# Kernel tuning notes

Hardware: AMD Instinct MI355X
Metric: run time of the kernel (lower is better)

The kernel has to match this reference:

```python
import jax, jax.numpy as jnp
import numpy as np

DOWN = 8
N_CLASSES = 80
IOU_THRESH = 0.7
ALL_ANCHORS = np.array([[10, 13], [16, 30], [33, 23], [30, 61], [62, 45],
                        [59, 119], [116, 90], [156, 198], [373, 326]],
                       np.float32) / DOWN              # anchors in grid units
ANCHOR_IDX = np.array([0, 1, 2])
ANCHORS = ALL_ANCHORS[ANCHOR_IDX]                       # [A,2]
A = 3
NC = N_CLASSES + 5


def _clog(z):
    # torch BCE clamps log at -100; double-where keeps grads finite at z==0
    safe = jnp.where(z > 0, z, 1.0)
    return jnp.where(z > 0, jnp.clip(jnp.log(safe), -100.0, None), -100.0)


def _bce_sum(p, t, w=None):
    term = t * _clog(p) + (1.0 - t) * _clog(1.0 - p)
    if w is not None:
        term = term * w
    return -jnp.sum(term)


def reference(x, targets, conv_w, conv_b):
    B, Cin, F, _ = x.shape
    T = targets.shape[1]
    anchors = jnp.asarray(ANCHORS)
    all_anchors = jnp.asarray(ALL_ANCHORS)

    # 1x1 conv + axis swap -> [B, A, Fy, Fx, NC]
    out = jnp.einsum('bchw,oc->bohw', x, conv_w) + conv_b[None, :, None, None]
    out = out.reshape(B, A, NC, F, F).transpose(0, 1, 3, 4, 2)
    sig = jax.nn.sigmoid(out)
    outputs = jnp.concatenate([sig[..., :2], out[..., 2:4], sig[..., 4:]], axis=-1)

    # decoded predicted boxes (detached), grid units
    gr = jnp.arange(F, dtype=outputs.dtype)
    grid = jnp.stack([jnp.broadcast_to(gr[None, :], (F, F)),
                      jnp.broadcast_to(gr[:, None], (F, F))], -1)   # (x,y)
    pred_xy = outputs[..., :2] + grid[None, None]
    pred_wh = jnp.exp(outputs[..., 2:4]) * anchors[None, :, None, None, :]
    pred_boxes = jax.lax.stop_gradient(jnp.concatenate([pred_xy, pred_wh], -1))

    # ground truth in grid units; valid targets are packed first (sum > 0)
    valid = jnp.sum(targets, axis=2) > 0                 # [B,T]
    n_t = jnp.sum(valid.astype(jnp.int32), axis=1)       # [B]
    gt_boxes = targets[..., :4] * F
    gt_cls = targets[..., 4].astype(jnp.int32)
    gxi = gt_boxes[..., 0].astype(jnp.int32)
    gyi = gt_boxes[..., 1].astype(jnp.int32)

    # best-matching anchor per gt (shape-only IoU vs all 9 anchors)
    wh = gt_boxes[..., 2:4]
    inter = jnp.prod(jnp.minimum(wh[:, :, None, :], all_anchors[None, None]), -1)
    union = (jnp.prod(wh, -1)[:, :, None]
             + jnp.prod(all_anchors, -1)[None, None] - inter)
    best = jnp.argmax(inter / (union + 1e-16), axis=2)   # [B,T]
    match = best[:, :, None] == jnp.asarray(ANCHOR_IDX)[None, None, :]
    keep = valid & jnp.any(match, -1)
    la = jnp.where(keep, jnp.argmax(match, -1), A)       # A == out-of-bounds -> drop

    # ignore predictions whose best IoU against any valid gt exceeds threshold
    p = pred_boxes.reshape(B, -1, 1, 4)                  # [B, A*F*F, 1, 4]
    g = gt_boxes[:, None, :, :]                          # [B, 1, T, 4]
    lo = jnp.maximum(p[..., :2] - p[..., 2:] * 0.5, g[..., :2] - g[..., 2:] * 0.5)
    hi = jnp.minimum(p[..., :2] + p[..., 2:] * 0.5, g[..., :2] + g[..., 2:] * 0.5)
    ia = jnp.prod(jnp.clip(hi - lo, 0.0, None), -1)
    iou = ia / (jnp.prod(p[..., 2:], -1) + jnp.prod(g[..., 2:], -1) - ia + 1e-16)
    iou = jnp.where(valid[:, None, :], iou, 0.0)
    high = (jnp.max(iou, -1) > IOU_THRESH).reshape(B, A, F, F).astype(outputs.dtype)
    a_rng = jnp.arange(A)
    object_mask = jnp.where(a_rng[None, :, None, None] < n_t[:, None, None, None],
                            1.0 - high, jnp.ones((), outputs.dtype))

    # scatter gt assignments (unique grid cells per image in setup -> no dup writes)
    bidx = jnp.broadcast_to(jnp.arange(B)[:, None], (B, T))
    anch = anchors[jnp.where(keep, la, 0)]               # [B,T,2]
    vals = jnp.concatenate([
        gt_boxes[..., :2] - jnp.floor(gt_boxes[..., :2]),           # frac xy
        jnp.log(gt_boxes[..., 2:4] / anch + 1e-16),                 # log wh
        jnp.ones((B, T, 1), outputs.dtype),                          # obj
        jax.nn.one_hot(gt_cls, N_CLASSES, dtype=outputs.dtype)], -1)
    scale_v = jnp.sqrt(2.0 - gt_boxes[..., 2] * gt_boxes[..., 3] / (F * F))

    tgt = jnp.zeros_like(outputs).at[bidx, la, gyi, gxi].set(vals, mode='drop')
    tmask = jnp.zeros((B, A, F, F), outputs.dtype).at[bidx, la, gyi, gxi].set(1.0, mode='drop')
    tscale = jnp.zeros((B, A, F, F), outputs.dtype).at[bidx, la, gyi, gxi].set(scale_v, mode='drop')
    object_mask = object_mask.at[bidx, la, gyi, gxi].set(1.0, mode='drop')

    tm = tmask[..., None]
    sm = tscale[..., None]
    loss_xy = _bce_sum(outputs[..., :2] * tm, tgt[..., :2] * tm, w=sm * sm)
    loss_wh = 0.5 * jnp.sum((outputs[..., 2:4] * tm * sm - tgt[..., 2:4] * tm * sm) ** 2)
    loss_obj = _bce_sum(outputs[..., 4] * object_mask, tgt[..., 4] * object_mask)
    loss_cls = _bce_sum(outputs[..., 5:] * tm, tgt[..., 5:] * tm)
    loss = loss_xy + loss_wh + loss_obj + loss_cls
    return loss, loss_xy, loss_wh, loss_obj, loss_cls


def setup_inputs():
    key = jax.random.key(0)
    k1, k2, k3 = jax.random.split(key, 3)
    B, Cin, F, T = 16, 256, 76, 50
    x = jax.random.normal(k1, (B, Cin, F, F), jnp.float32)
    conv_w = jax.random.normal(k2, (A * NC, Cin), jnp.float32) * 0.01
    conv_b = jax.random.normal(k3, (A * NC,), jnp.float32) * 0.01
    rng = np.random.default_rng(0)
    tg = np.zeros((B, T, 5), np.float32)
    for b in range(B):  # host-side data generation, not part of the op
        n = int(rng.integers(10, T + 1))
        cells = rng.choice(F * F, size=n, replace=False)   # unique grid cells
        gy, gx = cells // F, cells % F
        tg[b, :n, 0] = (gx + rng.uniform(0.05, 0.95, n)) / F
        tg[b, :n, 1] = (gy + rng.uniform(0.05, 0.95, n)) / F
        tg[b, :n, 2] = rng.uniform(0.02, 0.35, n)
        tg[b, :n, 3] = rng.uniform(0.02, 0.35, n)
        tg[b, :n, 4] = rng.integers(0, N_CLASSES, n)
    return {"x": x, "targets": jnp.asarray(tg), "conv_w": conv_w, "conv_b": conv_b}
```

## Files before the change

### kernel.cpp

```cpp
#include <hip/hip_runtime.h>
#include <math.h>

#define NB   16
#define CIN  256
#define FW   76
#define FF   (FW*FW)
#define NT   50
#define NA   3
#define NCH  85
#define POSB 256
#define NCONV ((FF + POSB - 1)/POSB)
#define CONV_BLOCKS (NB*NCONV)
#define TGT_BLOCKS  (NB*NT)

__device__ __constant__ float c_aw[9] = {1.25f,2.0f,4.125f,3.75f,7.75f,7.375f,14.5f,19.5f,46.625f};
__device__ __constant__ float c_ah[9] = {1.625f,3.75f,2.875f,7.625f,5.625f,14.875f,11.25f,24.75f,40.75f};

__device__ inline float clogf_(float z){
  return (z > 0.f) ? fmaxf(logf(z), -100.f) : -100.f;
}
__device__ inline float sigmoidf_(float z){
  return 1.f/(1.f + expf(-z));
}

struct TInfo {
  int valid, keep, la, gxi, gyi, cls;
  float gx, gy, gw, gh;
};

__device__ inline TInfo make_tinfo(const float* __restrict__ tg, int b, int t){
  const float* p = tg + ((size_t)b*NT + t)*5;
  float x=p[0], y=p[1], w=p[2], h=p[3], c=p[4];
  TInfo r;
  r.valid = (x+y+w+h+c) > 0.f ? 1 : 0;
  r.gx = x*(float)FW; r.gy = y*(float)FW; r.gw = w*(float)FW; r.gh = h*(float)FW;
  r.gxi = (int)r.gx; r.gyi = (int)r.gy;
  r.cls = (int)c;
  int best=0; float br=-1.f;
  #pragma unroll
  for (int i=0;i<9;++i){
    float inter = fminf(r.gw, c_aw[i]) * fminf(r.gh, c_ah[i]);
    float uni = r.gw*r.gh + c_aw[i]*c_ah[i] - inter;
    float rt = inter/(uni + 1e-16f);
    if (rt > br){ br = rt; best = i; }
  }
  r.la = best;
  r.keep = (r.valid && best < NA) ? 1 : 0;
  return r;
}

__global__ __launch_bounds__(256) void yolo_fused(
    const float* __restrict__ x, const float* __restrict__ tg,
    const float* __restrict__ W, const float* __restrict__ bias,
    double* __restrict__ accum)
{
  const int bid = blockIdx.x;
  const int tid = threadIdx.x;

  if (bid < CONV_BLOCKS) {
    const int b   = bid / NCONV;
    const int pos = (bid % NCONV)*POSB + tid;
    const bool act = pos < FF;
    const int posc = act ? pos : 0;

    __shared__ float s_x1[NT], s_y1[NT], s_x2[NT], s_y2[NT], s_area[NT];
    __shared__ int   s_val[NT], s_code[NT];
    __shared__ int   s_nt;
    __shared__ float s_red[POSB];

    int myvalid = 0;
    if (tid < NT) {
      TInfo ti = make_tinfo(tg, b, tid);
      myvalid = ti.valid;
      s_val[tid]  = ti.valid;
      s_x1[tid]   = ti.gx - 0.5f*ti.gw;
      s_x2[tid]   = ti.gx + 0.5f*ti.gw;
      s_y1[tid]   = ti.gy - 0.5f*ti.gh;
      s_y2[tid]   = ti.gy + 0.5f*ti.gh;
      s_area[tid] = ti.gw*ti.gh;
      s_code[tid] = ti.keep ? (ti.la*FF + ti.gyi*FW + ti.gxi) : -1;
    }
    if (tid < 64) {
      unsigned long long m = __ballot(myvalid != 0);
      if (tid == 0) s_nt = __popcll(m);
    }
    __syncthreads();

    float acc[NA][5];
    #pragma unroll
    for (int a=0;a<NA;++a)
      #pragma unroll
      for (int c=0;c<5;++c) acc[a][c] = 0.f;

    const float* __restrict__ xp = x + (size_t)b*CIN*FF + posc;
    for (int k0=0; k0<CIN; k0+=8) {
      float xv[8];
      #pragma unroll
      for (int j=0;j<8;++j) xv[j] = xp[(size_t)(k0+j)*FF];
      #pragma unroll
      for (int j=0;j<8;++j) {
        const int k = k0 + j;
        #pragma unroll
        for (int a=0;a<NA;++a)
          #pragma unroll
          for (int c=0;c<5;++c)
            acc[a][c] = fmaf(xv[j], W[(size_t)(a*NCH+c)*CIN + k], acc[a][c]);
      }
    }

    float lobj = 0.f;
    if (act) {
      const int gx = pos % FW;
      const int gy = pos / FW;
      #pragma unroll
      for (int a=0;a<NA;++a) {
        const float z0 = acc[a][0] + bias[a*NCH+0];
        const float z1 = acc[a][1] + bias[a*NCH+1];
        const float z2 = acc[a][2] + bias[a*NCH+2];
        const float z3 = acc[a][3] + bias[a*NCH+3];
        const float z4 = acc[a][4] + bias[a*NCH+4];
        const float s0 = sigmoidf_(z0);
        const float s1 = sigmoidf_(z1);
        const float s4 = sigmoidf_(z4);
        const float px = s0 + (float)gx;
        const float py = s1 + (float)gy;
        const float pw = expf(z2)*c_aw[a];
        const float ph = expf(z3)*c_ah[a];
        const float px1 = px - 0.5f*pw, px2 = px + 0.5f*pw;
        const float py1 = py - 0.5f*ph, py2 = py + 0.5f*ph;
        const float parea = pw*ph;
        bool high = false, ist = false;
        const int code = a*FF + pos;
        for (int t=0;t<NT;++t) {
          if (s_val[t]) {
            float iw = fminf(px2, s_x2[t]) - fmaxf(px1, s_x1[t]); iw = fmaxf(iw, 0.f);
            float ih = fminf(py2, s_y2[t]) - fmaxf(py1, s_y1[t]); ih = fmaxf(ih, 0.f);
            float ia = iw*ih;
            float iou = ia / (parea + s_area[t] - ia + 1e-16f);
            high = high || (iou > 0.7f);
          }
          ist = ist || (s_code[t] == code);
        }
        float mask = ist ? 1.f : ((a < s_nt) ? (high ? 0.f : 1.f) : 1.f);
        if (mask != 0.f)
          lobj -= ist ? clogf_(s4) : clogf_(1.f - s4);
      }
    }

    s_red[tid] = lobj;
    __syncthreads();
    #pragma unroll
    for (int s=POSB/2; s>0; s>>=1) {
      if (tid < s) s_red[tid] += s_red[tid+s];
      __syncthreads();
    }
    if (tid == 0) atomicAdd(accum+2, (double)s_red[0]);

  } else {
    const int idx = bid - CONV_BLOCKS;
    const int b = idx / NT, t = idx % NT;
    TInfo ti = make_tinfo(tg, b, t);
    if (!ti.keep) return;
    const int a   = ti.la;
    const int pos = ti.gyi*FW + ti.gxi;

    __shared__ float xs[CIN];
    __shared__ float sdot[NCH*3];
    __shared__ float sxy, swh, scls;
    if (tid == 0) { sxy = 0.f; swh = 0.f; scls = 0.f; }
    if (tid < CIN) xs[tid] = x[((size_t)b*CIN + tid)*FF + pos];
    __syncthreads();

    if (tid < NCH*3) {
      const int c = tid/3, ks = tid%3;
      const int kb = ks*86;
      const int ke = (kb+86 < CIN) ? kb+86 : CIN;
      const float* __restrict__ wr = W + (size_t)(a*NCH + c)*CIN;
      float p = 0.f;
      for (int k=kb;k<ke;++k) p = fmaf(xs[k], wr[k], p);
      sdot[tid] = p;
    }
    __syncthreads();

    if (tid < NCH) {
      const float z = sdot[tid*3] + sdot[tid*3+1] + sdot[tid*3+2] + bias[a*NCH + tid];
      const float scale = sqrtf(2.f - ti.gw*ti.gh/(float)(FW*FW));
      if (tid < 2) {
        const float tv = (tid==0) ? (ti.gx - floorf(ti.gx)) : (ti.gy - floorf(ti.gy));
        const float p  = sigmoidf_(z);
        const float term = tv*clogf_(p) + (1.f-tv)*clogf_(1.f-p);
        atomicAdd(&sxy, -term*scale*scale);
      } else if (tid < 4) {
        const float anch = (tid==2) ? c_aw[a] : c_ah[a];
        const float g    = (tid==2) ? ti.gw  : ti.gh;
        const float tv   = logf(g/anch + 1e-16f);
        const float d    = (z - tv)*scale;
        atomicAdd(&swh, 0.5f*d*d);
      } else if (tid >= 5) {
        const float tv = ((tid-5) == ti.cls) ? 1.f : 0.f;
        const float p  = sigmoidf_(z);
        const float term = tv*clogf_(p) + (1.f-tv)*clogf_(1.f-p);
        atomicAdd(&scls, -term);
      }
    }
    __syncthreads();
    if (tid == 0) {
      atomicAdd(accum+0, (double)sxy);
      atomicAdd(accum+1, (double)swh);
      atomicAdd(accum+3, (double)scls);
    }
  }
}

__global__ void yolo_init(double* __restrict__ accum){
  if (threadIdx.x < 4) accum[threadIdx.x] = 0.0;
}

__global__ void yolo_fin(const double* __restrict__ accum, float* __restrict__ out){
  if (threadIdx.x == 0) {
    float fxy  = (float)accum[0];
    float fwh  = (float)accum[1];
    float fobj = (float)accum[2];
    float fcls = (float)accum[3];
    out[0] = fxy + fwh + fobj + fcls;
    out[1] = fxy;
    out[2] = fwh;
    out[3] = fobj;
    out[4] = fcls;
  }
}

extern "C" void kernel_launch(void* const* d_in, const int* in_sizes, int n_in,
                              void* d_out, int out_size, void* d_ws, size_t ws_size,
                              hipStream_t stream) {
  const float* x    = (const float*)d_in[0];
  const float* tg   = (const float*)d_in[1];
  const float* W    = (const float*)d_in[2];
  const float* bias = (const float*)d_in[3];
  float*  out   = (float*)d_out;
  double* accum = (double*)d_ws;

  hipLaunchKernelGGL(yolo_init, dim3(1), dim3(64), 0, stream, accum);
  hipLaunchKernelGGL(yolo_fused, dim3(CONV_BLOCKS + TGT_BLOCKS), dim3(POSB), 0, stream,
                     x, tg, W, bias, accum);
  hipLaunchKernelGGL(yolo_fin, dim3(1), dim3(64), 0, stream, accum, out);
}
```

Measured before the change: 213.8 us.

## Double-buffer x tiles via global_load_lds and replace atomics with per-block partials

The conv loop now stages 32-channel slices of x into a double-buffered LDS tile using direct global-to-LDS loads, prefetching the next slice while computing the current one. Previously each thread loaded x straight from global memory with register batching. Double atomics into a shared accumulator are replaced by per-block partial sums that a 256-thread finish kernel reduces, which also removes the init kernel launch. The changes add 64 KB of LDS per block, which may lower occupancy, and a barrier per chunk.

```diff
diff --git a/kernel.cpp b/kernel.cpp
--- a/kernel.cpp
+++ b/kernel.cpp
@@ -12,6 +12,9 @@
 #define NCONV ((FF + POSB - 1)/POSB)
 #define CONV_BLOCKS (NB*NCONV)
 #define TGT_BLOCKS  (NB*NT)
+#define TOT_BLOCKS  (CONV_BLOCKS + TGT_BLOCKS)
+#define KT   32
+#define NCHUNK (CIN/KT)
 
 __device__ __constant__ float c_aw[9] = {1.25f,2.0f,4.125f,3.75f,7.75f,7.375f,14.5f,19.5f,46.625f};
 __device__ __constant__ float c_ah[9] = {1.625f,3.75f,2.875f,7.625f,5.625f,14.875f,11.25f,24.75f,40.75f};
@@ -21,6 +24,12 @@
 }
 __device__ inline float sigmoidf_(float z){
   return 1.f/(1.f + expf(-z));
+}
+
+__device__ __forceinline__ void gload_lds16(const float* src, float* dst){
+  __builtin_amdgcn_global_load_lds(
+      (const __attribute__((address_space(1))) void*)src,
+      (__attribute__((address_space(3))) void*)dst, 16, 0, 0);
 }
 
 struct TInfo {
@@ -52,21 +61,23 @@
 __global__ __launch_bounds__(256) void yolo_fused(
     const float* __restrict__ x, const float* __restrict__ tg,
     const float* __restrict__ W, const float* __restrict__ bias,
-    double* __restrict__ accum)
+    double* __restrict__ part)
 {
   const int bid = blockIdx.x;
   const int tid = threadIdx.x;
 
   if (bid < CONV_BLOCKS) {
-    const int b   = bid / NCONV;
-    const int pos = (bid % NCONV)*POSB + tid;
-    const bool act = pos < FF;
-    const int posc = act ? pos : 0;
-
+    __shared__ float xbuf[2][KT][POSB];
     __shared__ float s_x1[NT], s_y1[NT], s_x2[NT], s_y2[NT], s_area[NT];
     __shared__ int   s_val[NT], s_code[NT];
     __shared__ int   s_nt;
     __shared__ float s_red[POSB];
+
+    const int b    = bid / NCONV;
+    const int chunk= bid % NCONV;
+    const int pos0 = chunk*POSB;
+    const int pos  = pos0 + tid;
+    const bool act = pos < FF;
 
     int myvalid = 0;
     if (tid < NT) {
@@ -84,6 +95,18 @@
       unsigned long long m = __ballot(myvalid != 0);
       if (tid == 0) s_nt = __popcll(m);
     }
+
+    const int lane = tid & 63;
+    const int w    = tid >> 6;
+    int srcpos = pos0 + lane*4;
+    if (srcpos > FF-4) srcpos = FF-4;
+    const float* xsrc = x + (size_t)b*CIN*FF + srcpos;
+
+    #pragma unroll
+    for (int j=0;j<8;++j){
+      const int krow = w*8 + j;
+      gload_lds16(xsrc + (size_t)krow*FF, &xbuf[0][krow][0]);
+    }
     __syncthreads();
 
     float acc[NA][5];
@@ -92,20 +115,29 @@
       #pragma unroll
       for (int c=0;c<5;++c) acc[a][c] = 0.f;
 
-    const float* __restrict__ xp = x + (size_t)b*CIN*FF + posc;
-    for (int k0=0; k0<CIN; k0+=8) {
-      float xv[8];
-      #pragma unroll
-      for (int j=0;j<8;++j) xv[j] = xp[(size_t)(k0+j)*FF];
-      #pragma unroll
-      for (int j=0;j<8;++j) {
-        const int k = k0 + j;
+    int cb = 0;
+    for (int c=0;c<NCHUNK;++c){
+      if (c+1 < NCHUNK){
+        const int k0n = (c+1)*KT;
+        #pragma unroll
+        for (int j=0;j<8;++j){
+          const int krow = w*8 + j;
+          gload_lds16(xsrc + (size_t)(k0n+krow)*FF, &xbuf[cb^1][krow][0]);
+        }
+      }
+      const int k0 = c*KT;
+      #pragma unroll 8
+      for (int kk=0; kk<KT; ++kk){
+        const float xv = xbuf[cb][kk][tid];
+        const int k = k0 + kk;
         #pragma unroll
         for (int a=0;a<NA;++a)
           #pragma unroll
-          for (int c=0;c<5;++c)
-            acc[a][c] = fmaf(xv[j], W[(size_t)(a*NCH+c)*CIN + k], acc[a][c]);
-      }
+          for (int ch=0;ch<5;++ch)
+            acc[a][ch] = fmaf(xv, W[(size_t)(a*NCH+ch)*CIN + k], acc[a][ch]);
+      }
+      __syncthreads();
+      cb ^= 1;
     }
 
     float lobj = 0.f;
@@ -154,74 +186,88 @@
       if (tid < s) s_red[tid] += s_red[tid+s];
       __syncthreads();
     }
-    if (tid == 0) atomicAdd(accum+2, (double)s_red[0]);
+    if (tid == 0) {
+      double* p = part + (size_t)bid*4;
+      p[0] = 0.0; p[1] = 0.0; p[2] = (double)s_red[0]; p[3] = 0.0;
+    }
 
   } else {
     const int idx = bid - CONV_BLOCKS;
     const int b = idx / NT, t = idx % NT;
     TInfo ti = make_tinfo(tg, b, t);
-    if (!ti.keep) return;
-    const int a   = ti.la;
-    const int pos = ti.gyi*FW + ti.gxi;
 
     __shared__ float xs[CIN];
     __shared__ float sdot[NCH*3];
     __shared__ float sxy, swh, scls;
     if (tid == 0) { sxy = 0.f; swh = 0.f; scls = 0.f; }
-    if (tid < CIN) xs[tid] = x[((size_t)b*CIN + tid)*FF + pos];
-    __syncthreads();
-
-    if (tid < NCH*3) {
-      const int c = tid/3, ks = tid%3;
-      const int kb = ks*86;
-      const int ke = (kb+86 < CIN) ? kb+86 : CIN;
-      const float* __restrict__ wr = W + (size_t)(a*NCH + c)*CIN;
-      float p = 0.f;
-      for (int k=kb;k<ke;++k) p = fmaf(xs[k], wr[k], p);
-      sdot[tid] = p;
-    }
-    __syncthreads();
-
-    if (tid < NCH) {
-      const float z = sdot[tid*3] + sdot[tid*3+1] + sdot[tid*3+2] + bias[a*NCH + tid];
-      const float scale = sqrtf(2.f - ti.gw*ti.gh/(float)(FW*FW));
-      if (tid < 2) {
-        const float tv = (tid==0) ? (ti.gx - floorf(ti.gx)) : (ti.gy - floorf(ti.gy));
-        const float p  = sigmoidf_(z);
-        const float term = tv*clogf_(p) + (1.f-tv)*clogf_(1.f-p);
-        atomicAdd(&sxy, -term*scale*scale);
-      } else if (tid < 4) {
-        const float anch = (tid==2) ? c_aw[a] : c_ah[a];
-        const float g    = (tid==2) ? ti.gw  : ti.gh;
-        const float tv   = logf(g/anch + 1e-16f);
-        const float d    = (z - tv)*scale;
-        atomicAdd(&swh, 0.5f*d*d);
-      } else if (tid >= 5) {
-        const float tv = ((tid-5) == ti.cls) ? 1.f : 0.f;
-        const float p  = sigmoidf_(z);
-        const float term = tv*clogf_(p) + (1.f-tv)*clogf_(1.f-p);
-        atomicAdd(&scls, -term);
-      }
-    }
-    __syncthreads();
+    __syncthreads();
+
+    if (ti.keep) {
+      const int a   = ti.la;
+      const int pos = ti.gyi*FW + ti.gxi;
+      if (tid < CIN) xs[tid] = x[((size_t)b*CIN + tid)*FF + pos];
+      __syncthreads();
+
+      if (tid < NCH*3) {
+        const int c = tid/3, ks = tid%3;
+        const int kb = ks*86;
+        const int ke = (kb+86 < CIN) ? kb+86 : CIN;
+        const float* __restrict__ wr = W + (size_t)(a*NCH + c)*CIN;
+        float p = 0.f;
+        for (int k=kb;k<ke;++k) p = fmaf(xs[k], wr[k], p);
+        sdot[tid] = p;
+      }
+      __syncthreads();
+
+      if (tid < NCH) {
+        const float z = sdot[tid*3] + sdot[tid*3+1] + sdot[tid*3+2] + bias[a*NCH + tid];
+        const float scale = sqrtf(2.f - ti.gw*ti.gh/(float)(FW*FW));
+        if (tid < 2) {
+          const float tv = (tid==0) ? (ti.gx - floorf(ti.gx)) : (ti.gy - floorf(ti.gy));
+          const float p  = sigmoidf_(z);
+          const float term = tv*clogf_(p) + (1.f-tv)*clogf_(1.f-p);
+          atomicAdd(&sxy, -term*scale*scale);
+        } else if (tid < 4) {
+          const float anch = (tid==2) ? c_aw[a] : c_ah[a];
+          const float g    = (tid==2) ? ti.gw  : ti.gh;
+          const float tv   = logf(g/anch + 1e-16f);
+          const float d    = (z - tv)*scale;
+          atomicAdd(&swh, 0.5f*d*d);
+        } else if (tid >= 5) {
+          const float tv = ((tid-5) == ti.cls) ? 1.f : 0.f;
+          const float p  = sigmoidf_(z);
+          const float term = tv*clogf_(p) + (1.f-tv)*clogf_(1.f-p);
+          atomicAdd(&scls, -term);
+        }
+      }
+      __syncthreads();
+    }
+
     if (tid == 0) {
-      atomicAdd(accum+0, (double)sxy);
-      atomicAdd(accum+1, (double)swh);
-      atomicAdd(accum+3, (double)scls);
-    }
-  }
-}
-
-__global__ void yolo_init(double* __restrict__ accum){
-  if (threadIdx.x < 4) accum[threadIdx.x] = 0.0;
-}
-
-__global__ void yolo_fin(const double* __restrict__ accum, float* __restrict__ out){
-  if (threadIdx.x == 0) {
-    float fxy  = (float)accum[0];
-    float fwh  = (float)accum[1];
-    float fobj = (float)accum[2];
-    float fcls = (float)accum[3];
+      double* p = part + (size_t)bid*4;
+      p[0] = (double)sxy; p[1] = (double)swh; p[2] = 0.0; p[3] = (double)scls;
+    }
+  }
+}
+
+__global__ void yolo_fin(const double* __restrict__ part, float* __restrict__ out){
+  __shared__ double red[256];
+  const int tid = threadIdx.x;
+  double s = 0.0;
+  for (int i = tid>>2; i < TOT_BLOCKS; i += 64)
+    s += part[(size_t)i*4 + (tid&3)];
+  red[tid] = s;
+  __syncthreads();
+  #pragma unroll
+  for (int st=128; st>=4; st>>=1) {
+    if (tid < st) red[tid] += red[tid+st];
+    __syncthreads();
+  }
+  if (tid == 0) {
+    float fxy  = (float)red[0];
+    float fwh  = (float)red[1];
+    float fobj = (float)red[2];
+    float fcls = (float)red[3];
     out[0] = fxy + fwh + fobj + fcls;
     out[1] = fxy;
     out[2] = fwh;
@@ -237,11 +283,10 @@
   const float* tg   = (const float*)d_in[1];
   const float* W    = (const float*)d_in[2];
   const float* bias = (const float*)d_in[3];
-  float*  out   = (float*)d_out;
-  double* accum = (double*)d_ws;
-
-  hipLaunchKernelGGL(yolo_init, dim3(1), dim3(64), 0, stream, accum);
-  hipLaunchKernelGGL(yolo_fused, dim3(CONV_BLOCKS + TGT_BLOCKS), dim3(POSB), 0, stream,
-                     x, tg, W, bias, accum);
-  hipLaunchKernelGGL(yolo_fin, dim3(1), dim3(64), 0, stream, accum, out);
-}
+  float*  out  = (float*)d_out;
+  double* part = (double*)d_ws;
+
+  hipLaunchKernelGGL(yolo_fused, dim3(TOT_BLOCKS), dim3(POSB), 0, stream,
+                     x, tg, W, bias, part);
+  hipLaunchKernelGGL(yolo_fin, dim3(1), dim3(256), 0, stream, part, out);
+}
```

Result: faster. 207.3 us (-3.0%).
